# Performance work log

Measured on AMD Instinct MI355X. Metric: run time of the kernel, lower is better.

The kernel has to match this reference:

```python
import jax, jax.numpy as jnp
import numpy as np

K = 512           # num_embeddings
D = 256           # embedding_dim
GRID = (16, 32)   # SOM grid, prod == K
SIGMA = 2.0       # Gaussian neighborhood width (blur at step 0)
COMMITMENT_COST = 0.25
KOHONEN_COST = 1.0


def _make_blur_matrix():
    # Grid.init id->coord: coord[j] = (i // prod(shape[:j])) % shape[j]
    idx = np.arange(K)
    c0 = idx % GRID[0]
    c1 = (idx // GRID[0]) % GRID[1]
    coords = np.stack([c0, c1], axis=-1).astype(np.float32)  # [K, 2]
    dist = np.linalg.norm(coords[None, :, :] - coords[:, None, :], axis=-1)  # [K, K]
    return jnp.asarray(np.exp(-(dist ** 2) / (2.0 * SIGMA ** 2)), dtype=jnp.float32)


def setup_inputs() -> dict:
    key = jax.random.key(0)
    kx, kw = jax.random.split(key)
    x = jax.random.normal(kx, (64, 32, 32, D), dtype=jnp.float32)
    w = jax.random.normal(kw, (K, D), dtype=jnp.float32)
    bmat = _make_blur_matrix()  # [K, K] constant buffer
    return {"x": x, "w": w, "bmat": bmat}


def reference(x, w, bmat):
    sg = jax.lax.stop_gradient
    flat = x.reshape(-1, D)  # [N, D]

    # nearest-code search (no_grad in torch)
    fw = sg(flat)
    ww = sg(w)
    dists = (jnp.sum(fw ** 2, axis=1, keepdims=True)
             + jnp.sum(ww ** 2, axis=1)
             - 2.0 * fw @ ww.T)                       # [N, K]
    enc_idx = jnp.argmin(dists, axis=1)               # [N]
    encodings = jax.nn.one_hot(enc_idx, K, dtype=jnp.float32)  # [N, K]

    # embedding lookup (differentiable w.r.t. w)
    quant_flat = w[enc_idx]                           # [N, D]
    quantized = quant_flat.reshape(x.shape)

    # l2_batch(w, quantized.detach()) -> [N, K]
    qd = sg(quant_flat)
    diff = (jnp.sum(w ** 2, axis=1)[None, :]
            + jnp.sum(qd ** 2, axis=1, keepdims=True)
            - 2.0 * qd @ w.T)                         # [N, K]

    # blur-weighted kohonen loss: bmm(diff[N,1,K], bmat[idx][N,K,1]).mean()
    selected = bmat[enc_idx]                          # [N, K]
    kohonen_loss = jnp.mean(jnp.sum(diff * selected, axis=-1))

    avg_probs = jnp.mean(encodings, axis=0)
    perplexity = jnp.exp(-jnp.sum(avg_probs * jnp.log(avg_probs + 1e-10)))

    e_latent = jnp.mean((sg(quantized) - x) ** 2)
    q_latent = jnp.mean((quantized - sg(x)) ** 2)
    loss = q_latent + COMMITMENT_COST * e_latent + KOHONEN_COST * kohonen_loss

    quantized_st = x + sg(quantized - x)              # straight-through
    return loss, quantized_st, perplexity, enc_idx
```

## Files before the change

### kernel.cpp

```cpp
#include <hip/hip_runtime.h>
#include <hip/hip_bf16.h>
#include <hip/hip_fp16.h>
#include <math.h>

#define NPTS 65536
#define DIM  256
#define KC   512

#define BM    64
#define NBLK  (NPTS / BM)
#define XSTR  264
#define EPS   0.01f

#define QOFF  1
#define PIDX  16777217
#define EOFF  16777218


typedef _Float16 h8    __attribute__((ext_vector_type(8)));
typedef float    f32x4 __attribute__((ext_vector_type(4)));

__device__ inline void cvt_split8(float4 a, float4 b, h8& hv, h8& lv) {
    float f[8] = {a.x, a.y, a.z, a.w, b.x, b.y, b.z, b.w};
    #pragma unroll
    for (int i = 0; i < 8; ++i) {
        _Float16 h = (_Float16)f[i];
        hv[i] = h;
        lv[i] = (_Float16)(f[i] - (float)h);
    }
}

__device__ inline void merge_top2(float& b1, int& i1, float& b2, int& i2,
                                  float ob1, int oi1, float ob2, int oi2) {
    bool ow = (ob1 < b1) || (ob1 == b1 && oi1 < i1);
    float lb = ow ? b1 : ob1; int li = ow ? i1 : oi1;
    if (ow) { b1 = ob1; i1 = oi1; }
    float c2 = b2; int ci = i2;
    if (ob2 < c2 || (ob2 == c2 && oi2 < ci)) { c2 = ob2; ci = oi2; }
    if (lb  < c2 || (lb  == c2 && li  < ci)) { c2 = lb;  ci = li;  }
    b2 = c2; i2 = ci;
}

__device__ inline float exact_dist(const float* __restrict__ xr,
                                   const float* __restrict__ w, int c, float wsqc) {
    const float* wr = w + (size_t)c * DIM;
    float d0 = 0.f, d1 = 0.f, d2 = 0.f, d3 = 0.f;
    #pragma unroll 4
    for (int d = 0; d < DIM; d += 4) {
        d0 = fmaf(xr[d + 0], wr[d + 0], d0);
        d1 = fmaf(xr[d + 1], wr[d + 1], d1);
        d2 = fmaf(xr[d + 2], wr[d + 2], d2);
        d3 = fmaf(xr[d + 3], wr[d + 3], d3);
    }
    return wsqc - 2.f * ((d0 + d1) + (d2 + d3));
}

__global__ __launch_bounds__(256) void som_wsq(const float* __restrict__ w,
                                               float* __restrict__ wsq,
                                               int* __restrict__ hist,
                                               double* __restrict__ mse_acc)
{
    int k = blockIdx.x * 256 + threadIdx.x;
    const float4* r = reinterpret_cast<const float4*>(w + (size_t)k * DIM);
    float s0 = 0.f, s1 = 0.f, s2 = 0.f, s3 = 0.f;
    #pragma unroll 8
    for (int q = 0; q < DIM / 4; ++q) {
        float4 v = r[q];
        s0 = fmaf(v.x, v.x, s0);
        s1 = fmaf(v.y, v.y, s1);
        s2 = fmaf(v.z, v.z, s2);
        s3 = fmaf(v.w, v.w, s3);
    }
    wsq[k] = (s0 + s1) + (s2 + s3);
    hist[k] = 0;
    if (k == 0) *mse_acc = 0.0;
}

__global__ __launch_bounds__(256) void som_conv(const float* __restrict__ w,
                                                _Float16* __restrict__ wfh,
                                                _Float16* __restrict__ wfl)
{
    const int tid = threadIdx.x;
    const int row = blockIdx.x * 8 + (tid >> 5);
    const int g   = tid & 31;
    const float4* r = reinterpret_cast<const float4*>(w + (size_t)row * DIM);
    float4 a = r[g * 2], b = r[g * 2 + 1];
    h8 hv, lv; cvt_split8(a, b, hv, lv);
    int dsl = g >> 2, kg = g & 3;
    int ctg = row >> 4, l15 = row & 15;
    size_t off = (((size_t)(ctg * 8 + dsl)) * 4 + kg) * 128 + l15 * 8;
    *reinterpret_cast<h8*>(wfh + off) = hv;
    *reinterpret_cast<h8*>(wfl + off) = lv;
}

__global__ __launch_bounds__(512) void som_main(const float* __restrict__ x,
                                                const float* __restrict__ w,
                                                const _Float16* __restrict__ wfh,
                                                const _Float16* __restrict__ wfl,
                                                float* __restrict__ out,
                                                const float* __restrict__ wsq,
                                                int* __restrict__ hist,
                                                double* __restrict__ mse_acc)
{
    alignas(16) __shared__ _Float16 xh[BM * XSTR];
    alignas(16) __shared__ _Float16 xl[BM * XSTR];
    __shared__ float wsq_s[KC];
    __shared__ float red_b[8][BM], red_s[8][BM];
    __shared__ int   red_ib[8][BM], red_is[8][BM];
    __shared__ int   bidx_s[BM];
    __shared__ float wsum[8];

    const int tid  = threadIdx.x;
    const int lane = tid & 63;
    const int wid  = tid >> 6;
    const int l15  = lane & 15;
    const int kg   = lane >> 4;
    const int ptBlock = blockIdx.x * BM;

    const float4* xg4 = reinterpret_cast<const float4*>(x);
    #pragma unroll
    for (int it = 0; it < 4; ++it) {
        int u = it * 512 + tid;
        int row = u >> 5, c8 = u & 31;
        float4 a = xg4[(size_t)(ptBlock + row) * 64 + c8 * 2];
        float4 b = xg4[(size_t)(ptBlock + row) * 64 + c8 * 2 + 1];
        h8 hv, lv; cvt_split8(a, b, hv, lv);
        *reinterpret_cast<h8*>(&xh[row * XSTR + c8 * 8]) = hv;
        *reinterpret_cast<h8*>(&xl[row * XSTR + c8 * 8]) = lv;
    }
    wsq_s[tid] = wsq[tid];
    __syncthreads();

    float sb[4], ss[4];
    int   ib[4], is2[4];
    #pragma unroll
    for (int ct = 0; ct < 4; ++ct) { sb[ct] = INFINITY; ss[ct] = INFINITY; ib[ct] = 0; is2[ct] = 0; }

    const int codeBase = wid * 64;

    f32x4 acc[4][4];
    #pragma unroll
    for (int rt = 0; rt < 4; ++rt)
        #pragma unroll
        for (int ct = 0; ct < 4; ++ct)
            acc[rt][ct] = (f32x4){0.f, 0.f, 0.f, 0.f};

    #pragma unroll 1
    for (int dsl = 0; dsl < 8; ++dsl) {
        h8 Bh[4], Bl[4];
        #pragma unroll
        for (int ct = 0; ct < 4; ++ct) {
            int off = (ct * 16 + l15) * XSTR + dsl * 32 + kg * 8;
            Bh[ct] = *reinterpret_cast<const h8*>(&xh[off]);
            Bl[ct] = *reinterpret_cast<const h8*>(&xl[off]);
        }
        #pragma unroll
        for (int rt = 0; rt < 4; ++rt) {
            int ctg = (codeBase >> 4) + rt;
            size_t off = (((size_t)ctg * 8 + dsl) * 4 + kg) * 128 + l15 * 8;
            h8 Ah = *reinterpret_cast<const h8*>(wfh + off);
            h8 Al = *reinterpret_cast<const h8*>(wfl + off);
            #pragma unroll
            for (int ct = 0; ct < 4; ++ct)
                acc[rt][ct] = __builtin_amdgcn_mfma_f32_16x16x32_f16(Ah, Bh[ct], acc[rt][ct], 0, 0, 0);
            #pragma unroll
            for (int ct = 0; ct < 4; ++ct)
                acc[rt][ct] = __builtin_amdgcn_mfma_f32_16x16x32_f16(Al, Bh[ct], acc[rt][ct], 0, 0, 0);
            #pragma unroll
            for (int ct = 0; ct < 4; ++ct)
                acc[rt][ct] = __builtin_amdgcn_mfma_f32_16x16x32_f16(Ah, Bl[ct], acc[rt][ct], 0, 0, 0);
        }
    }

    #pragma unroll
    for (int rt = 0; rt < 4; ++rt) {
        int cbase = codeBase + rt * 16 + kg * 4;
        #pragma unroll
        for (int ct = 0; ct < 4; ++ct) {
            #pragma unroll
            for (int r = 0; r < 4; ++r) {
                int c = cbase + r;
                float d = wsq_s[c] - 2.f * acc[rt][ct][r];
                if (d < sb[ct] || (d == sb[ct] && c < ib[ct])) {
                    ss[ct] = sb[ct]; is2[ct] = ib[ct]; sb[ct] = d; ib[ct] = c;
                } else if (d < ss[ct] || (d == ss[ct] && c < is2[ct])) {
                    ss[ct] = d; is2[ct] = c;
                }
            }
        }
    }

    #pragma unroll
    for (int ct = 0; ct < 4; ++ct) {
        #pragma unroll
        for (int m = 16; m <= 32; m <<= 1) {
            float ob1 = __shfl_xor(sb[ct], m, 64), ob2 = __shfl_xor(ss[ct], m, 64);
            int   oi1 = __shfl_xor(ib[ct], m, 64), oi2 = __shfl_xor(is2[ct], m, 64);
            merge_top2(sb[ct], ib[ct], ss[ct], is2[ct], ob1, oi1, ob2, oi2);
        }
    }
    if (kg == 0) {
        #pragma unroll
        for (int ct = 0; ct < 4; ++ct) {
            int p = ct * 16 + l15;
            red_b[wid][p] = sb[ct];  red_s[wid][p] = ss[ct];
            red_ib[wid][p] = ib[ct]; red_is[wid][p] = is2[ct];
        }
    }
    __syncthreads();

    if (tid < BM) {
        float b = red_b[0][tid], s = red_s[0][tid];
        int  bi = red_ib[0][tid], si = red_is[0][tid];
        #pragma unroll
        for (int g = 1; g < 8; ++g)
            merge_top2(b, bi, s, si, red_b[g][tid], red_ib[g][tid], red_s[g][tid], red_is[g][tid]);

        if (s - b < EPS) {
            const float* xr = x + (size_t)(ptBlock + tid) * DIM;
            float d1 = exact_dist(xr, w, bi, wsq_s[bi]);
            float d2 = exact_dist(xr, w, si, wsq_s[si]);
            if (d2 < d1 || (d2 == d1 && si < bi)) bi = si;
        }
        bidx_s[tid] = bi;
        out[EOFF + ptBlock + tid] = (float)bi;
        atomicAdd(&hist[bi], 1);
    }
    __syncthreads();

    {
        int d = tid & 255;
        int ph = tid >> 8;
        float lsum = 0.f;
        for (int pp = 0; pp < BM / 2; ++pp) {
            int p = pp * 2 + ph;
            int c = bidx_s[p];
            float qv = w[(size_t)c * DIM + d];
            float xv = x[(size_t)(ptBlock + p) * DIM + d];
            out[QOFF + (size_t)(ptBlock + p) * DIM + d] = qv;
            float dd = qv - xv;
            lsum = fmaf(dd, dd, lsum);
        }
        #pragma unroll
        for (int m = 32; m; m >>= 1) lsum += __shfl_xor(lsum, m, 64);
        if (lane == 0) wsum[wid] = lsum;
    }
    __syncthreads();
    if (tid == 0) {
        float t = 0.f;
        #pragma unroll
        for (int i = 0; i < 8; ++i) t += wsum[i];
        atomicAdd(mse_acc, (double)t);
    }
}

__global__ __launch_bounds__(256) void som_g(const float* __restrict__ w,
                                             const float* __restrict__ bmat,
                                             const float* __restrict__ wsq,
                                             float* __restrict__ g)
{
    __shared__ float wj[DIM];
    __shared__ float psum[4];
    const int j = blockIdx.x;
    const int tid = threadIdx.x;
    wj[tid] = w[(size_t)j * DIM + tid];
    __syncthreads();
    const float wsqj = wsq[j];
    float sum = 0.f;
    for (int k = tid; k < KC; k += 256) {
        const float* wk = &w[(size_t)k * DIM];
        float d0 = 0.f, d1 = 0.f, d2 = 0.f, d3 = 0.f;
        #pragma unroll 4
        for (int d = 0; d < DIM; d += 4) {
            d0 = fmaf(wj[d + 0], wk[d + 0], d0);
            d1 = fmaf(wj[d + 1], wk[d + 1], d1);
            d2 = fmaf(wj[d + 2], wk[d + 2], d2);
            d3 = fmaf(wj[d + 3], wk[d + 3], d3);
        }
        float dot = (d0 + d1) + (d2 + d3);
        float t = wsq[k] + wsqj - 2.f * dot;
        sum = fmaf(bmat[(size_t)j * KC + k], t, sum);
    }
    #pragma unroll
    for (int m = 32; m; m >>= 1) sum += __shfl_xor(sum, m, 64);
    int lane = tid & 63, wid = tid >> 6;
    if (lane == 0) psum[wid] = sum;
    __syncthreads();
    if (tid == 0) g[j] = (psum[0] + psum[1]) + (psum[2] + psum[3]);
}

__global__ __launch_bounds__(512) void som_final(const int* __restrict__ hist,
                                                 const float* __restrict__ g,
                                                 const double* __restrict__ mse_acc,
                                                 float* __restrict__ out)
{
    __shared__ float e_part[8], k_part[8];
    const int tid = threadIdx.x;
    int cnt = hist[tid];
    float p = (float)cnt / (float)NPTS;
    float ent = -p * logf(p + 1e-10f);
    float koh = (float)cnt * g[tid];
    #pragma unroll
    for (int m = 32; m; m >>= 1) {
        ent += __shfl_xor(ent, m, 64);
        koh += __shfl_xor(koh, m, 64);
    }
    int lane = tid & 63, wid = tid >> 6;
    if (lane == 0) { e_part[wid] = ent; k_part[wid] = koh; }
    __syncthreads();
    if (tid == 0) {
        float es = 0.f, ks = 0.f;
        #pragma unroll
        for (int i = 0; i < 8; ++i) { es += e_part[i]; ks += k_part[i]; }
        float mse = (float)(*mse_acc / (double)(NPTS * (size_t)DIM));
        out[0] = fmaf(1.25f, mse, ks / (float)NPTS);
        out[PIDX] = expf(es);
    }
}

extern "C" void kernel_launch(void* const* d_in, const int* in_sizes, int n_in,
                              void* d_out, int out_size, void* d_ws, size_t ws_size,
                              hipStream_t stream) {
    const float* x    = (const float*)d_in[0];
    const float* w    = (const float*)d_in[1];
    const float* bmat = (const float*)d_in[2];
    float* out = (float*)d_out;

    _Float16* wfh = (_Float16*)d_ws;
    _Float16* wfl = wfh + 131072;
    float*  wsq  = (float*)((char*)d_ws + 524288);
    float*  g    = (float*)((char*)d_ws + 526336);
    int*    hist = (int*)((char*)d_ws + 528384);
    double* mse  = (double*)((char*)d_ws + 530432);

    som_wsq  <<<2, 256, 0, stream>>>(w, wsq, hist, mse);
    som_conv <<<64, 256, 0, stream>>>(w, wfh, wfl);
    som_main <<<NBLK, 512, 0, stream>>>(x, w, wfh, wfl, out, wsq, hist, mse);
    som_g    <<<KC, 256, 0, stream>>>(w, bmat, wsq, g);
    som_final<<<1, KC, 0, stream>>>(hist, g, mse, out);
}
```

Measured before the change: 163.4 us.

## Split quantized gather into separate kernel, derive MSE algebraically, prefetch codebook fragments

The main kernel no longer re-reads x and w per point to write quantized rows and accumulate MSE. Instead it computes each point's squared norm while staging x, and adds it to the winning distance to get the MSE term. A new som_quant kernel gathers codebook rows into the output with float4 accesses, using the stored indices. The MFMA loop now double-buffers the fp16 hi/lo codebook fragments in registers so global loads overlap compute. The trade-offs are higher register pressure, an extra launch, reliance on the approximate distance for the MSE when the top-2 refinement is skipped, and float4 stores at an offset of one float.

```diff
diff --git a/kernel.cpp b/kernel.cpp
--- a/kernel.cpp
+++ b/kernel.cpp
@@ -93,6 +93,28 @@
     *reinterpret_cast<h8*>(wfl + off) = lv;
 }
 
+#define MFMA_PHASE(dslv, AH, AL) do {                                                     \
+    h8 Bh[4], Bl[4];                                                                      \
+    _Pragma("unroll")                                                                     \
+    for (int ct = 0; ct < 4; ++ct) {                                                      \
+        int boff = (ct * 16 + l15) * XSTR + (dslv) * 32 + kg * 8;                         \
+        Bh[ct] = *reinterpret_cast<const h8*>(&xh[boff]);                                 \
+        Bl[ct] = *reinterpret_cast<const h8*>(&xl[boff]);                                 \
+    }                                                                                     \
+    _Pragma("unroll")                                                                     \
+    for (int rt = 0; rt < 4; ++rt) {                                                      \
+        _Pragma("unroll")                                                                 \
+        for (int ct = 0; ct < 4; ++ct)                                                    \
+            acc[rt][ct] = __builtin_amdgcn_mfma_f32_16x16x32_f16(AH[rt], Bh[ct], acc[rt][ct], 0, 0, 0); \
+        _Pragma("unroll")                                                                 \
+        for (int ct = 0; ct < 4; ++ct)                                                    \
+            acc[rt][ct] = __builtin_amdgcn_mfma_f32_16x16x32_f16(AL[rt], Bh[ct], acc[rt][ct], 0, 0, 0); \
+        _Pragma("unroll")                                                                 \
+        for (int ct = 0; ct < 4; ++ct)                                                    \
+            acc[rt][ct] = __builtin_amdgcn_mfma_f32_16x16x32_f16(AH[rt], Bl[ct], acc[rt][ct], 0, 0, 0); \
+    }                                                                                     \
+} while (0)
+
 __global__ __launch_bounds__(512) void som_main(const float* __restrict__ x,
                                                 const float* __restrict__ w,
                                                 const _Float16* __restrict__ wfh,
@@ -105,10 +127,9 @@
     alignas(16) __shared__ _Float16 xh[BM * XSTR];
     alignas(16) __shared__ _Float16 xl[BM * XSTR];
     __shared__ float wsq_s[KC];
+    __shared__ float xsq_s[BM];
     __shared__ float red_b[8][BM], red_s[8][BM];
     __shared__ int   red_ib[8][BM], red_is[8][BM];
-    __shared__ int   bidx_s[BM];
-    __shared__ float wsum[8];
 
     const int tid  = threadIdx.x;
     const int lane = tid & 63;
@@ -127,50 +148,61 @@
         h8 hv, lv; cvt_split8(a, b, hv, lv);
         *reinterpret_cast<h8*>(&xh[row * XSTR + c8 * 8]) = hv;
         *reinterpret_cast<h8*>(&xl[row * XSTR + c8 * 8]) = lv;
+        float s = ((fmaf(a.x, a.x, a.y * a.y) + fmaf(a.z, a.z, a.w * a.w))
+                 + (fmaf(b.x, b.x, b.y * b.y) + fmaf(b.z, b.z, b.w * b.w)));
+        #pragma unroll
+        for (int m = 1; m <= 16; m <<= 1) s += __shfl_xor(s, m, 64);
+        if ((lane & 31) == 0) xsq_s[row] = s;
     }
     wsq_s[tid] = wsq[tid];
     __syncthreads();
+
+    const int codeBase = wid * 64;
+    const int ctg0 = codeBase >> 4;
+    const int lane_off = kg * 128 + l15 * 8;
+    const _Float16* __restrict__ pH = wfh + lane_off;
+    const _Float16* __restrict__ pL = wfl + lane_off;
+
+    f32x4 acc[4][4];
+    #pragma unroll
+    for (int rt = 0; rt < 4; ++rt)
+        #pragma unroll
+        for (int ct = 0; ct < 4; ++ct)
+            acc[rt][ct] = (f32x4){0.f, 0.f, 0.f, 0.f};
+
+    h8 Ah0[4], Al0[4], Ah1[4], Al1[4];
+    #pragma unroll
+    for (int rt = 0; rt < 4; ++rt) {
+        size_t off = ((size_t)((ctg0 + rt) * 8 + 0)) * 512;
+        Ah0[rt] = *reinterpret_cast<const h8*>(pH + off);
+        Al0[rt] = *reinterpret_cast<const h8*>(pL + off);
+    }
+
+    #pragma unroll 1
+    for (int ds2 = 0; ds2 < 4; ++ds2) {
+        const int dA = ds2 * 2, dB = dA + 1;
+        #pragma unroll
+        for (int rt = 0; rt < 4; ++rt) {
+            size_t off = ((size_t)((ctg0 + rt) * 8 + dB)) * 512;
+            Ah1[rt] = *reinterpret_cast<const h8*>(pH + off);
+            Al1[rt] = *reinterpret_cast<const h8*>(pL + off);
+        }
+        MFMA_PHASE(dA, Ah0, Al0);
+        if (ds2 < 3) {
+            #pragma unroll
+            for (int rt = 0; rt < 4; ++rt) {
+                size_t off = ((size_t)((ctg0 + rt) * 8 + dA + 2)) * 512;
+                Ah0[rt] = *reinterpret_cast<const h8*>(pH + off);
+                Al0[rt] = *reinterpret_cast<const h8*>(pL + off);
+            }
+        }
+        MFMA_PHASE(dB, Ah1, Al1);
+    }
 
     float sb[4], ss[4];
     int   ib[4], is2[4];
     #pragma unroll
     for (int ct = 0; ct < 4; ++ct) { sb[ct] = INFINITY; ss[ct] = INFINITY; ib[ct] = 0; is2[ct] = 0; }
-
-    const int codeBase = wid * 64;
-
-    f32x4 acc[4][4];
-    #pragma unroll
-    for (int rt = 0; rt < 4; ++rt)
-        #pragma unroll
-        for (int ct = 0; ct < 4; ++ct)
-            acc[rt][ct] = (f32x4){0.f, 0.f, 0.f, 0.f};
-
-    #pragma unroll 1
-    for (int dsl = 0; dsl < 8; ++dsl) {
-        h8 Bh[4], Bl[4];
-        #pragma unroll
-        for (int ct = 0; ct < 4; ++ct) {
-            int off = (ct * 16 + l15) * XSTR + dsl * 32 + kg * 8;
-            Bh[ct] = *reinterpret_cast<const h8*>(&xh[off]);
-            Bl[ct] = *reinterpret_cast<const h8*>(&xl[off]);
-        }
-        #pragma unroll
-        for (int rt = 0; rt < 4; ++rt) {
-            int ctg = (codeBase >> 4) + rt;
-            size_t off = (((size_t)ctg * 8 + dsl) * 4 + kg) * 128 + l15 * 8;
-            h8 Ah = *reinterpret_cast<const h8*>(wfh + off);
-            h8 Al = *reinterpret_cast<const h8*>(wfl + off);
-            #pragma unroll
-            for (int ct = 0; ct < 4; ++ct)
-                acc[rt][ct] = __builtin_amdgcn_mfma_f32_16x16x32_f16(Ah, Bh[ct], acc[rt][ct], 0, 0, 0);
-            #pragma unroll
-            for (int ct = 0; ct < 4; ++ct)
-                acc[rt][ct] = __builtin_amdgcn_mfma_f32_16x16x32_f16(Al, Bh[ct], acc[rt][ct], 0, 0, 0);
-            #pragma unroll
-            for (int ct = 0; ct < 4; ++ct)
-                acc[rt][ct] = __builtin_amdgcn_mfma_f32_16x16x32_f16(Ah, Bl[ct], acc[rt][ct], 0, 0, 0);
-        }
-    }
 
     #pragma unroll
     for (int rt = 0; rt < 4; ++rt) {
@@ -220,37 +252,31 @@
             const float* xr = x + (size_t)(ptBlock + tid) * DIM;
             float d1 = exact_dist(xr, w, bi, wsq_s[bi]);
             float d2 = exact_dist(xr, w, si, wsq_s[si]);
-            if (d2 < d1 || (d2 == d1 && si < bi)) bi = si;
-        }
-        bidx_s[tid] = bi;
+            if (d2 < d1 || (d2 == d1 && si < bi)) { bi = si; b = d2; } else { b = d1; }
+        }
         out[EOFF + ptBlock + tid] = (float)bi;
         atomicAdd(&hist[bi], 1);
-    }
-    __syncthreads();
-
-    {
-        int d = tid & 255;
-        int ph = tid >> 8;
-        float lsum = 0.f;
-        for (int pp = 0; pp < BM / 2; ++pp) {
-            int p = pp * 2 + ph;
-            int c = bidx_s[p];
-            float qv = w[(size_t)c * DIM + d];
-            float xv = x[(size_t)(ptBlock + p) * DIM + d];
-            out[QOFF + (size_t)(ptBlock + p) * DIM + d] = qv;
-            float dd = qv - xv;
-            lsum = fmaf(dd, dd, lsum);
-        }
-        #pragma unroll
-        for (int m = 32; m; m >>= 1) lsum += __shfl_xor(lsum, m, 64);
-        if (lane == 0) wsum[wid] = lsum;
-    }
-    __syncthreads();
-    if (tid == 0) {
-        float t = 0.f;
-        #pragma unroll
-        for (int i = 0; i < 8; ++i) t += wsum[i];
-        atomicAdd(mse_acc, (double)t);
+
+        float msum = xsq_s[tid] + b;
+        #pragma unroll
+        for (int m = 32; m; m >>= 1) msum += __shfl_xor(msum, m, 64);
+        if (tid == 0) atomicAdd(mse_acc, (double)msum);
+    }
+}
+
+__global__ __launch_bounds__(256) void som_quant(const float* __restrict__ w,
+                                                 float* __restrict__ out)
+{
+    const int tid = threadIdx.x;
+    const int d4  = tid & 63;
+    const int rg  = tid >> 6;
+    const float4* wg4 = reinterpret_cast<const float4*>(w);
+    float4* q4 = reinterpret_cast<float4*>(out + QOFF);
+    #pragma unroll
+    for (int it = 0; it < 4; ++it) {
+        int row = blockIdx.x * 16 + it * 4 + rg;
+        int c = (int)out[EOFF + row];
+        q4[(size_t)row * 64 + d4] = wg4[(size_t)c * 64 + d4];
     }
 }
 
@@ -336,6 +362,7 @@
     som_wsq  <<<2, 256, 0, stream>>>(w, wsq, hist, mse);
     som_conv <<<64, 256, 0, stream>>>(w, wfh, wfl);
     som_main <<<NBLK, 512, 0, stream>>>(x, w, wfh, wfl, out, wsq, hist, mse);
+    som_quant<<<4096, 256, 0, stream>>>(w, out);
     som_g    <<<KC, 256, 0, stream>>>(w, bmat, wsq, g);
     som_final<<<1, KC, 0, stream>>>(hist, g, mse, out);
 }
```

After: 182.2 us. 1.11x slower.

## Process four point tiles per block with double-buffered x staging and algebraic MSE

Applied to the files above, without the earlier changes.

Each block now handles four 64-point tiles instead of one. The next tile's x is prefetched into registers and converted into a second LDS buffer while the current tile is being finished, which overlaps global loads with compute. The MSE term is now derived algebraically from the per-point x norm plus the best distance, so the separate reread of x in the epilogue goes away. The quantized-row copy uses float4 stores. In exchange the kernel launches fewer blocks and uses more LDS, and the MSE now depends on the accuracy of the fp16-split distance for points that skip the exact recheck.

```diff
diff --git a/kernel.cpp b/kernel.cpp
--- a/kernel.cpp
+++ b/kernel.cpp
@@ -8,7 +8,8 @@
 #define KC   512
 
 #define BM    64
-#define NBLK  (NPTS / BM)
+#define NTILE 4
+#define NBLK  256
 #define XSTR  264
 #define EPS   0.01f
 
@@ -102,155 +103,177 @@
                                                 int* __restrict__ hist,
                                                 double* __restrict__ mse_acc)
 {
-    alignas(16) __shared__ _Float16 xh[BM * XSTR];
-    alignas(16) __shared__ _Float16 xl[BM * XSTR];
+    alignas(16) __shared__ _Float16 xh[2][BM * XSTR];
+    alignas(16) __shared__ _Float16 xl[2][BM * XSTR];
     __shared__ float wsq_s[KC];
+    __shared__ float xsq_s[2][BM];
     __shared__ float red_b[8][BM], red_s[8][BM];
     __shared__ int   red_ib[8][BM], red_is[8][BM];
     __shared__ int   bidx_s[BM];
-    __shared__ float wsum[8];
 
     const int tid  = threadIdx.x;
     const int lane = tid & 63;
     const int wid  = tid >> 6;
     const int l15  = lane & 15;
     const int kg   = lane >> 4;
-    const int ptBlock = blockIdx.x * BM;
+    const int tile0 = blockIdx.x * NTILE;
+
+    wsq_s[tid] = wsq[tid];
 
     const float4* xg4 = reinterpret_cast<const float4*>(x);
-    #pragma unroll
-    for (int it = 0; it < 4; ++it) {
-        int u = it * 512 + tid;
-        int row = u >> 5, c8 = u & 31;
-        float4 a = xg4[(size_t)(ptBlock + row) * 64 + c8 * 2];
-        float4 b = xg4[(size_t)(ptBlock + row) * 64 + c8 * 2 + 1];
-        h8 hv, lv; cvt_split8(a, b, hv, lv);
-        *reinterpret_cast<h8*>(&xh[row * XSTR + c8 * 8]) = hv;
-        *reinterpret_cast<h8*>(&xl[row * XSTR + c8 * 8]) = lv;
-    }
-    wsq_s[tid] = wsq[tid];
+    const float4* wg4 = reinterpret_cast<const float4*>(w);
+    float4* q4 = reinterpret_cast<float4*>(out + QOFF);
+
+    float4 xr[4][2];
+
+    auto loadx = [&](int tt) {
+        #pragma unroll
+        for (int it = 0; it < 4; ++it) {
+            int u = it * 512 + tid, row = u >> 5, c8 = u & 31;
+            size_t base = (size_t)(tt * BM + row) * 64 + c8 * 2;
+            xr[it][0] = xg4[base];
+            xr[it][1] = xg4[base + 1];
+        }
+    };
+    auto cvtwrite = [&](int c) {
+        #pragma unroll
+        for (int it = 0; it < 4; ++it) {
+            int u = it * 512 + tid, row = u >> 5, c8 = u & 31;
+            h8 hv, lv; cvt_split8(xr[it][0], xr[it][1], hv, lv);
+            *reinterpret_cast<h8*>(&xh[c][row * XSTR + c8 * 8]) = hv;
+            *reinterpret_cast<h8*>(&xl[c][row * XSTR + c8 * 8]) = lv;
+            float4 a = xr[it][0], b = xr[it][1];
+            float s = ((fmaf(a.x, a.x, a.y * a.y) + fmaf(a.z, a.z, a.w * a.w))
+                     + (fmaf(b.x, b.x, b.y * b.y) + fmaf(b.z, b.z, b.w * b.w)));
+            #pragma unroll
+            for (int m = 1; m <= 16; m <<= 1) s += __shfl_xor(s, m, 64);
+            if ((lane & 31) == 0) xsq_s[c][row] = s;
+        }
+    };
+
+    loadx(tile0);
+    cvtwrite(0);
+    loadx(tile0 + 1);
     __syncthreads();
 
-    float sb[4], ss[4];
-    int   ib[4], is2[4];
-    #pragma unroll
-    for (int ct = 0; ct < 4; ++ct) { sb[ct] = INFINITY; ss[ct] = INFINITY; ib[ct] = 0; is2[ct] = 0; }
-
     const int codeBase = wid * 64;
-
-    f32x4 acc[4][4];
-    #pragma unroll
-    for (int rt = 0; rt < 4; ++rt)
-        #pragma unroll
-        for (int ct = 0; ct < 4; ++ct)
-            acc[rt][ct] = (f32x4){0.f, 0.f, 0.f, 0.f};
+    const int ctg0 = codeBase >> 4;
+    const _Float16* __restrict__ pH = wfh + kg * 128 + l15 * 8;
+    const _Float16* __restrict__ pL = wfl + kg * 128 + l15 * 8;
 
     #pragma unroll 1
-    for (int dsl = 0; dsl < 8; ++dsl) {
-        h8 Bh[4], Bl[4];
+    for (int t = 0; t < NTILE; ++t) {
+        const int c = t & 1;
+        const int ptBlock = (tile0 + t) * BM;
+        const _Float16* __restrict__ bxh = xh[c];
+        const _Float16* __restrict__ bxl = xl[c];
+
+        f32x4 acc[4][4];
+        #pragma unroll
+        for (int rt = 0; rt < 4; ++rt)
+            #pragma unroll
+            for (int ct = 0; ct < 4; ++ct)
+                acc[rt][ct] = (f32x4){0.f, 0.f, 0.f, 0.f};
+
+        #pragma unroll 1
+        for (int dsl = 0; dsl < 8; ++dsl) {
+            h8 Bh[4], Bl[4];
+            #pragma unroll
+            for (int ct = 0; ct < 4; ++ct) {
+                int boff = (ct * 16 + l15) * XSTR + dsl * 32 + kg * 8;
+                Bh[ct] = *reinterpret_cast<const h8*>(&bxh[boff]);
+                Bl[ct] = *reinterpret_cast<const h8*>(&bxl[boff]);
+            }
+            #pragma unroll
+            for (int rt = 0; rt < 4; ++rt) {
+                size_t aoff = ((size_t)((ctg0 + rt) * 8 + dsl)) * 512;
+                h8 Ah = *reinterpret_cast<const h8*>(pH + aoff);
+                h8 Al = *reinterpret_cast<const h8*>(pL + aoff);
+                #pragma unroll
+                for (int ct = 0; ct < 4; ++ct)
+                    acc[rt][ct] = __builtin_amdgcn_mfma_f32_16x16x32_f16(Ah, Bh[ct], acc[rt][ct], 0, 0, 0);
+                #pragma unroll
+                for (int ct = 0; ct < 4; ++ct)
+                    acc[rt][ct] = __builtin_amdgcn_mfma_f32_16x16x32_f16(Al, Bh[ct], acc[rt][ct], 0, 0, 0);
+                #pragma unroll
+                for (int ct = 0; ct < 4; ++ct)
+                    acc[rt][ct] = __builtin_amdgcn_mfma_f32_16x16x32_f16(Ah, Bl[ct], acc[rt][ct], 0, 0, 0);
+            }
+        }
+
+        float sb[4], ss[4];
+        int   ib[4], is2[4];
+        #pragma unroll
+        for (int ct = 0; ct < 4; ++ct) { sb[ct] = INFINITY; ss[ct] = INFINITY; ib[ct] = 0; is2[ct] = 0; }
+        #pragma unroll
+        for (int rt = 0; rt < 4; ++rt) {
+            int cbase = codeBase + rt * 16 + kg * 4;
+            #pragma unroll
+            for (int ct = 0; ct < 4; ++ct) {
+                #pragma unroll
+                for (int r = 0; r < 4; ++r) {
+                    int cc = cbase + r;
+                    float d = wsq_s[cc] - 2.f * acc[rt][ct][r];
+                    if (d < sb[ct] || (d == sb[ct] && cc < ib[ct])) {
+                        ss[ct] = sb[ct]; is2[ct] = ib[ct]; sb[ct] = d; ib[ct] = cc;
+                    } else if (d < ss[ct] || (d == ss[ct] && cc < is2[ct])) {
+                        ss[ct] = d; is2[ct] = cc;
+                    }
+                }
+            }
+        }
         #pragma unroll
         for (int ct = 0; ct < 4; ++ct) {
-            int off = (ct * 16 + l15) * XSTR + dsl * 32 + kg * 8;
-            Bh[ct] = *reinterpret_cast<const h8*>(&xh[off]);
-            Bl[ct] = *reinterpret_cast<const h8*>(&xl[off]);
-        }
-        #pragma unroll
-        for (int rt = 0; rt < 4; ++rt) {
-            int ctg = (codeBase >> 4) + rt;
-            size_t off = (((size_t)ctg * 8 + dsl) * 4 + kg) * 128 + l15 * 8;
-            h8 Ah = *reinterpret_cast<const h8*>(wfh + off);
-            h8 Al = *reinterpret_cast<const h8*>(wfl + off);
-            #pragma unroll
-            for (int ct = 0; ct < 4; ++ct)
-                acc[rt][ct] = __builtin_amdgcn_mfma_f32_16x16x32_f16(Ah, Bh[ct], acc[rt][ct], 0, 0, 0);
-            #pragma unroll
-            for (int ct = 0; ct < 4; ++ct)
-                acc[rt][ct] = __builtin_amdgcn_mfma_f32_16x16x32_f16(Al, Bh[ct], acc[rt][ct], 0, 0, 0);
-            #pragma unroll
-            for (int ct = 0; ct < 4; ++ct)
-                acc[rt][ct] = __builtin_amdgcn_mfma_f32_16x16x32_f16(Ah, Bl[ct], acc[rt][ct], 0, 0, 0);
-        }
-    }
-
-    #pragma unroll
-    for (int rt = 0; rt < 4; ++rt) {
-        int cbase = codeBase + rt * 16 + kg * 4;
-        #pragma unroll
-        for (int ct = 0; ct < 4; ++ct) {
-            #pragma unroll
-            for (int r = 0; r < 4; ++r) {
-                int c = cbase + r;
-                float d = wsq_s[c] - 2.f * acc[rt][ct][r];
-                if (d < sb[ct] || (d == sb[ct] && c < ib[ct])) {
-                    ss[ct] = sb[ct]; is2[ct] = ib[ct]; sb[ct] = d; ib[ct] = c;
-                } else if (d < ss[ct] || (d == ss[ct] && c < is2[ct])) {
-                    ss[ct] = d; is2[ct] = c;
-                }
-            }
-        }
-    }
-
-    #pragma unroll
-    for (int ct = 0; ct < 4; ++ct) {
-        #pragma unroll
-        for (int m = 16; m <= 32; m <<= 1) {
-            float ob1 = __shfl_xor(sb[ct], m, 64), ob2 = __shfl_xor(ss[ct], m, 64);
-            int   oi1 = __shfl_xor(ib[ct], m, 64), oi2 = __shfl_xor(is2[ct], m, 64);
-            merge_top2(sb[ct], ib[ct], ss[ct], is2[ct], ob1, oi1, ob2, oi2);
-        }
-    }
-    if (kg == 0) {
-        #pragma unroll
-        for (int ct = 0; ct < 4; ++ct) {
-            int p = ct * 16 + l15;
-            red_b[wid][p] = sb[ct];  red_s[wid][p] = ss[ct];
-            red_ib[wid][p] = ib[ct]; red_is[wid][p] = is2[ct];
-        }
-    }
-    __syncthreads();
-
-    if (tid < BM) {
-        float b = red_b[0][tid], s = red_s[0][tid];
-        int  bi = red_ib[0][tid], si = red_is[0][tid];
-        #pragma unroll
-        for (int g = 1; g < 8; ++g)
-            merge_top2(b, bi, s, si, red_b[g][tid], red_ib[g][tid], red_s[g][tid], red_is[g][tid]);
-
-        if (s - b < EPS) {
-            const float* xr = x + (size_t)(ptBlock + tid) * DIM;
-            float d1 = exact_dist(xr, w, bi, wsq_s[bi]);
-            float d2 = exact_dist(xr, w, si, wsq_s[si]);
-            if (d2 < d1 || (d2 == d1 && si < bi)) bi = si;
-        }
-        bidx_s[tid] = bi;
-        out[EOFF + ptBlock + tid] = (float)bi;
-        atomicAdd(&hist[bi], 1);
-    }
-    __syncthreads();
-
-    {
-        int d = tid & 255;
-        int ph = tid >> 8;
-        float lsum = 0.f;
-        for (int pp = 0; pp < BM / 2; ++pp) {
-            int p = pp * 2 + ph;
-            int c = bidx_s[p];
-            float qv = w[(size_t)c * DIM + d];
-            float xv = x[(size_t)(ptBlock + p) * DIM + d];
-            out[QOFF + (size_t)(ptBlock + p) * DIM + d] = qv;
-            float dd = qv - xv;
-            lsum = fmaf(dd, dd, lsum);
-        }
-        #pragma unroll
-        for (int m = 32; m; m >>= 1) lsum += __shfl_xor(lsum, m, 64);
-        if (lane == 0) wsum[wid] = lsum;
-    }
-    __syncthreads();
-    if (tid == 0) {
-        float t = 0.f;
-        #pragma unroll
-        for (int i = 0; i < 8; ++i) t += wsum[i];
-        atomicAdd(mse_acc, (double)t);
+            #pragma unroll
+            for (int m = 16; m <= 32; m <<= 1) {
+                float ob1 = __shfl_xor(sb[ct], m, 64), ob2 = __shfl_xor(ss[ct], m, 64);
+                int   oi1 = __shfl_xor(ib[ct], m, 64), oi2 = __shfl_xor(is2[ct], m, 64);
+                merge_top2(sb[ct], ib[ct], ss[ct], is2[ct], ob1, oi1, ob2, oi2);
+            }
+        }
+        if (kg == 0) {
+            #pragma unroll
+            for (int ct = 0; ct < 4; ++ct) {
+                int p = ct * 16 + l15;
+                red_b[wid][p] = sb[ct];  red_s[wid][p] = ss[ct];
+                red_ib[wid][p] = ib[ct]; red_is[wid][p] = is2[ct];
+            }
+        }
+        __syncthreads();
+
+        if (tid < BM) {
+            float b = red_b[0][tid], s = red_s[0][tid];
+            int  bi = red_ib[0][tid], si = red_is[0][tid];
+            #pragma unroll
+            for (int g = 1; g < 8; ++g)
+                merge_top2(b, bi, s, si, red_b[g][tid], red_ib[g][tid], red_s[g][tid], red_is[g][tid]);
+
+            if (s - b < EPS) {
+                const float* xrp = x + (size_t)(ptBlock + tid) * DIM;
+                float d1 = exact_dist(xrp, w, bi, wsq_s[bi]);
+                float d2 = exact_dist(xrp, w, si, wsq_s[si]);
+                if (d2 < d1 || (d2 == d1 && si < bi)) { bi = si; b = d2; } else { b = d1; }
+            }
+            bidx_s[tid] = bi;
+            out[EOFF + ptBlock + tid] = (float)bi;
+            atomicAdd(&hist[bi], 1);
+
+            float msum = xsq_s[c][tid] + b;
+            #pragma unroll
+            for (int m = 32; m; m >>= 1) msum += __shfl_xor(msum, m, 64);
+            if (tid == 0) atomicAdd(mse_acc, (double)msum);
+        }
+        __syncthreads();
+
+        #pragma unroll
+        for (int r8 = 0; r8 < 8; ++r8) {
+            int row = r8 * 8 + wid;
+            int cc = bidx_s[row];
+            q4[(size_t)(ptBlock + row) * 64 + lane] = wg4[(size_t)cc * 64 + lane];
+        }
+        if (t + 1 < NTILE) cvtwrite(c ^ 1);
+        if (t + 2 < NTILE) loadx(tile0 + t + 2);
+        __syncthreads();
     }
 }
 
```

Result: slower. 182.1 us (+11.4%).
